# Optimization experiments

Hardware: AMD Instinct MI355X
Metric: run time of the kernel (lower is better)

## Reference

```python
import jax, jax.numpy as jnp
import numpy as np

NHEAD = 8
STRIP = 7  # strip_width (horizontal strips, is_vertical=False)


def setup_inputs() -> dict:
    key = jax.random.key(0)
    k0, k1, k2 = jax.random.split(key, 3)
    B, H, W, C = 2, 112, 112, 256
    x = jax.random.normal(k0, (B, H * W, C), dtype=jnp.float32)
    # torch nn.Linear weights: (out_features, in_features)
    qkv_w = jax.random.normal(k1, (3 * C, C), dtype=jnp.float32) * 0.02
    proj_w = jax.random.normal(k2, (C, C), dtype=jnp.float32) * 0.02
    proj_b = jnp.zeros((C,), dtype=jnp.float32)
    return {"x": x, "qkv_w": qkv_w, "proj_w": proj_w, "proj_b": proj_b,
            "H_feat": 112, "W_feat": 112}


def reference(x, qkv_w, proj_w, proj_b, H_feat, W_feat):
    B, N, C = x.shape
    hd = C // NHEAD
    scale = hd ** -0.5
    n_strips = H_feat // STRIP
    L = STRIP * W_feat  # tokens per horizontal strip
    # window_partition with window (STRIP, W_feat): nwW==1, so a pure reshape
    xs = x.reshape(B * n_strips, L, C)
    # qkv projection (Linear: y = x @ W^T), then split q/k/v and heads
    qkv = jnp.einsum('bnc,dc->bnd', xs, qkv_w)
    qkv = qkv.reshape(B * n_strips, L, 3, NHEAD, hd)
    q, k, v = jnp.moveaxis(qkv, 2, 0)  # each (Bw, L, H, hd)
    attn = jnp.einsum('bnhd,bmhd->bhnm', q * scale, k)
    attn = jax.nn.softmax(attn, axis=-1)
    out = jnp.einsum('bhnm,bmhd->bnhd', attn, v).reshape(B * n_strips, L, C)
    out = jnp.einsum('bnc,dc->bnd', out, proj_w) + proj_b
    # window_reverse is again a pure reshape for horizontal strips
    return out.reshape(B, N, C)
```

## Files before the change

### kernel.cpp

```cpp
#include <hip/hip_runtime.h>
#include <hip/hip_bf16.h>

#define M_ROWS 25088
#define CDIM   256
#define QKVD   768
#define LWIN   784
#define NWINH  256

typedef __attribute__((ext_vector_type(8))) short short8v;
typedef __attribute__((ext_vector_type(4))) float floatx4;

static __device__ __forceinline__ float bfs2f(unsigned short s) {
    return __uint_as_float(((unsigned int)s) << 16);
}
static __device__ __forceinline__ unsigned short f2bf(float f) {
    unsigned int x = __float_as_uint(f);
    x += 0x7fffu + ((x >> 16) & 1u);
    return (unsigned short)(x >> 16);
}
static __device__ __forceinline__ unsigned int cvt_pk_bf16(float a, float b) {
    unsigned int r;
    asm("v_cvt_pk_bf16_f32 %0, %1, %2" : "=v"(r) : "v"(a), "v"(b));
    return r;
}
static __device__ __forceinline__ void gld_lds16(const unsigned short* g,
                                                 unsigned short* l) {
    __builtin_amdgcn_global_load_lds(
        (const __attribute__((address_space(1))) unsigned int*)g,
        (__attribute__((address_space(3))) unsigned int*)l, 16, 0, 0);
}

__global__ __launch_bounds__(256) void k_f2bf(
    const float* __restrict__ src, unsigned short* __restrict__ dst, int n8)
{
    const float4* s4 = (const float4*)src;
    uint4* d4 = (uint4*)dst;
    for (int i = blockIdx.x * 256 + threadIdx.x; i < n8;
         i += gridDim.x * 256) {
        float4 a = s4[2 * i], b = s4[2 * i + 1];
        uint4 o;
        o.x = cvt_pk_bf16(a.x, a.y);
        o.y = cvt_pk_bf16(a.z, a.w);
        o.z = cvt_pk_bf16(b.x, b.y);
        o.w = cvt_pk_bf16(b.z, b.w);
        d4[i] = o;
    }
}

template <typename OUT_T, bool BIAS>
__global__ __launch_bounds__(256, 2) void k_gemm_mfma(
    const unsigned short* __restrict__ A,
    const unsigned short* __restrict__ B,
    const float* __restrict__ bias,
    OUT_T* __restrict__ Y, int N)
{
    __shared__ __attribute__((aligned(16))) unsigned short As[128 * 64];
    __shared__ __attribute__((aligned(16))) unsigned short Bs[128 * 64];
    const int t = threadIdx.x;
    const int lane = t & 63, wv = t >> 6;
    const int lq = lane & 15, g = lane >> 4;
    const int wm = wv >> 1, wn = wv & 1;
    const int R0 = blockIdx.y * 128, C0 = blockIdx.x * 128;
    const int lrow = t >> 3, lch = (t & 7) * 8;

    floatx4 acc[4][4];
#pragma unroll
    for (int i = 0; i < 4; ++i)
#pragma unroll
        for (int j = 0; j < 4; ++j) acc[i][j] = (floatx4){0.f, 0.f, 0.f, 0.f};

    for (int kc = 0; kc < 256; kc += 64) {
#pragma unroll
        for (int i = 0; i < 4; ++i) {
            gld_lds16(A + (size_t)(R0 + i * 32 + lrow) * 256 + kc + lch,
                      As + (i * 32 + wv * 8) * 64);
            gld_lds16(B + (size_t)(C0 + i * 32 + lrow) * 256 + kc + lch,
                      Bs + (i * 32 + wv * 8) * 64);
        }
        __syncthreads();
#pragma unroll
        for (int kk = 0; kk < 64; kk += 32) {
            short8v af[4], bf[4];
#pragma unroll
            for (int mi = 0; mi < 4; ++mi)
                af[mi] = *(const short8v*)(As + (wm * 64 + mi * 16 + lq) * 64 +
                                           kk + g * 8);
#pragma unroll
            for (int ni = 0; ni < 4; ++ni)
                bf[ni] = *(const short8v*)(Bs + (wn * 64 + ni * 16 + lq) * 64 +
                                           kk + g * 8);
#pragma unroll
            for (int mi = 0; mi < 4; ++mi)
#pragma unroll
                for (int ni = 0; ni < 4; ++ni)
                    acc[mi][ni] = __builtin_amdgcn_mfma_f32_16x16x32_bf16(
                        af[mi], bf[ni], acc[mi][ni], 0, 0, 0);
        }
        __syncthreads();
    }

#pragma unroll
    for (int mi = 0; mi < 4; ++mi) {
        const size_t rb = (size_t)R0 + wm * 64 + mi * 16 + g * 4;
#pragma unroll
        for (int ni = 0; ni < 4; ++ni) {
            const int col = C0 + wn * 64 + ni * 16 + lq;
            float bv = 0.f;
            if constexpr (BIAS) bv = bias[col];
#pragma unroll
            for (int r = 0; r < 4; ++r) {
                float val = acc[mi][ni][r] + bv;
                if constexpr (sizeof(OUT_T) == 2)
                    Y[(rb + r) * N + col] = (OUT_T)f2bf(val);
                else
                    Y[(rb + r) * N + col] = (OUT_T)val;
            }
        }
    }
}

#define VTP 808
#define KS_SZ (LWIN * 32)
#define VT_SZ (32 * VTP)
#define PB_OFF (KS_SZ + VT_SZ)
#define ATTN_LDS ((PB_OFF + 8 * 1280) * 2)

__global__ __launch_bounds__(512, 1) void k_attn_mfma(
    const unsigned short* __restrict__ qkv,
    unsigned short* __restrict__ ao)
{
    extern __shared__ unsigned short sm[];
    unsigned short* Ks = sm;
    unsigned short* Vt = sm + KS_SZ;
    const int t = threadIdx.x;
    const int lane = t & 63, wave = t >> 6;
    const int lq = lane & 15, g = lane >> 4;
    const int h = blockIdx.x & 7, w = blockIdx.x >> 3;
    const size_t rowbase = (size_t)w * LWIN;
    const unsigned short* base = qkv + rowbase * QKVD;

    for (int idx = t; idx < LWIN * 4; idx += 512) {
        const int row = idx >> 2, c = idx & 3;
        const size_t rb = (size_t)row * QKVD;
        uint4 kv = *(const uint4*)(base + rb + 256 + h * 32 + c * 8);
        *(uint4*)(Ks + c * (LWIN * 8) + row * 8) = kv;
        union { uint4 u; unsigned short s[8]; } vv;
        vv.u = *(const uint4*)(base + rb + 512 + h * 32 + c * 8);
#pragma unroll
        for (int j = 0; j < 8; ++j) Vt[(c * 8 + j) * VTP + row] = vv.s[j];
    }
    for (int idx = t; idx < 32 * 24; idx += 512) {
        Vt[(idx / 24) * VTP + LWIN + (idx % 24)] = 0;
    }
    __syncthreads();

    unsigned short* Pw = sm + PB_OFF + wave * 1280;
    const float CE = 1.4426950408889634f * 0.17677669529663687f;

    for (int c = wave; c < 25; c += 8) {
        const int tile0 = c * 2;
        const int nt = (c == 24) ? 1 : 2;
        short8v qf[2];
#pragma unroll
        for (int n = 0; n < 2; ++n)
            if (n < nt)
                qf[n] = *(const short8v*)(base +
                        (size_t)((tile0 + n) * 16 + lq) * QKVD + h * 32 + g * 8);

        floatx4 oa[2][2] = {{{0.f,0.f,0.f,0.f},{0.f,0.f,0.f,0.f}},
                            {{0.f,0.f,0.f,0.f},{0.f,0.f,0.f,0.f}}};
        float lsum[2] = {0.f, 0.f};

        auto do_score = [&](int s) {
            short8v kf = *(const short8v*)(Ks + g * (LWIN * 8) +
                                           (size_t)(s * 16 + lq) * 8);
#pragma unroll
            for (int n = 0; n < 2; ++n) {
                if (n < nt) {
                    floatx4 st = __builtin_amdgcn_mfma_f32_16x16x32_bf16(
                        kf, qf[n], (floatx4){0.f, 0.f, 0.f, 0.f}, 0, 0, 0);
                    float p0 = __builtin_amdgcn_exp2f(st[0] * CE);
                    float p1 = __builtin_amdgcn_exp2f(st[1] * CE);
                    float p2 = __builtin_amdgcn_exp2f(st[2] * CE);
                    float p3 = __builtin_amdgcn_exp2f(st[3] * CE);
                    lsum[n] += (p0 + p1) + (p2 + p3);
                    uint2 pw;
                    pw.x = cvt_pk_bf16(p0, p1);
                    pw.y = cvt_pk_bf16(p2, p3);
                    *(uint2*)(Pw + n * 640 + lq * 40 + (s & 1) * 16 + g * 4) = pw;
                }
            }
        };
        auto do_pv = [&](int tokbase) {
            short8v v0 = *(const short8v*)(Vt + (size_t)lq * VTP + tokbase + g * 8);
            short8v v1 = *(const short8v*)(Vt + (size_t)(lq + 16) * VTP + tokbase + g * 8);
#pragma unroll
            for (int n = 0; n < 2; ++n) {
                if (n < nt) {
                    short8v pf = *(const short8v*)(Pw + n * 640 + lq * 40 + g * 8);
                    oa[n][0] = __builtin_amdgcn_mfma_f32_16x16x32_bf16(
                        pf, v0, oa[n][0], 0, 0, 0);
                    oa[n][1] = __builtin_amdgcn_mfma_f32_16x16x32_bf16(
                        pf, v1, oa[n][1], 0, 0, 0);
                }
            }
        };

        for (int u = 0; u < 24; ++u) {
            do_score(2 * u);
            do_score(2 * u + 1);
            do_pv(u * 32);
        }
        do_score(48);
#pragma unroll
        for (int n = 0; n < 2; ++n) {
            if (n < nt) {
                uint2 z; z.x = 0u; z.y = 0u;
                *(uint2*)(Pw + n * 640 + lq * 40 + 16 + g * 4) = z;
            }
        }
        do_pv(768);

#pragma unroll
        for (int n = 0; n < 2; ++n) {
            if (n < nt) {
                float l = lsum[n];
                l += __shfl_xor(l, 16);
                l += __shfl_xor(l, 32);
                float inv = 1.f / l;
                const size_t orow0 = rowbase + (size_t)(tile0 + n) * 16;
#pragma unroll
                for (int r = 0; r < 4; ++r) {
                    float ir = __shfl(inv, (lane & 48) | (g * 4 + r));
                    size_t ob = (orow0 + g * 4 + r) * CDIM + h * 32;
                    ao[ob + lq]      = f2bf(oa[n][0][r] * ir);
                    ao[ob + 16 + lq] = f2bf(oa[n][1][r] * ir);
                }
            }
        }
    }
}

extern "C" void kernel_launch(void* const* d_in, const int* in_sizes, int n_in,
                              void* d_out, int out_size, void* d_ws, size_t ws_size,
                              hipStream_t stream) {
    const float* x      = (const float*)d_in[0];
    const float* qkv_w  = (const float*)d_in[1];
    const float* proj_w = (const float*)d_in[2];
    const float* proj_b = (const float*)d_in[3];
    float* out = (float*)d_out;

    unsigned short* qkvb = (unsigned short*)d_ws;
    unsigned short* xb   = qkvb + (size_t)M_ROWS * QKVD;
    unsigned short* aob  = xb;
    unsigned short* wqb  = xb + (size_t)M_ROWS * CDIM;
    unsigned short* wpb  = wqb + (size_t)QKVD * CDIM;

    hipFuncSetAttribute((const void*)k_attn_mfma,
                        hipFuncAttributeMaxDynamicSharedMemorySize, ATTN_LDS);

    k_f2bf<<<2048, 256, 0, stream>>>(x, xb, (M_ROWS * CDIM) / 8);
    k_f2bf<<<96, 256, 0, stream>>>(qkv_w, wqb, (QKVD * CDIM) / 8);
    k_f2bf<<<32, 256, 0, stream>>>(proj_w, wpb, (CDIM * CDIM) / 8);

    k_gemm_mfma<unsigned short, false>
        <<<dim3(QKVD / 128, M_ROWS / 128), 256, 0, stream>>>(
            xb, wqb, nullptr, qkvb, QKVD);

    k_attn_mfma<<<dim3(NWINH), 512, ATTN_LDS, stream>>>(qkvb, aob);

    k_gemm_mfma<float, true>
        <<<dim3(CDIM / 128, M_ROWS / 128), 256, 0, stream>>>(
            aob, wpb, proj_b, out, CDIM);
}
```

Measured before the change: 98.70 us.

## Use 16 waves per attention block with pair-packed V transpose and pre-scaled Q

The attention kernel now launches 1024 threads, and each of 16 waves handles one 16-row query tile instead of two tiles per wave across 8 waves. The score/PV loop is software-pipelined with a double-buffered P tile. V is transposed into LDS as 32-bit token pairs, which halves the scattered 16-bit LDS stores. The softmax scale times log2(e) is folded into the Q columns in the QKV GEMM epilogue, which removes a multiply per score. The cost is more LDS per block, higher register pressure under the 1024-thread bound, and Q being rounded to bf16 after scaling.

```diff
diff --git a/kernel.cpp b/kernel.cpp
--- a/kernel.cpp
+++ b/kernel.cpp
@@ -9,6 +9,8 @@
 
 typedef __attribute__((ext_vector_type(8))) short short8v;
 typedef __attribute__((ext_vector_type(4))) float floatx4;
+
+#define CEQ 0.2550660106245232f
 
 static __device__ __forceinline__ float bfs2f(unsigned short s) {
     return __uint_as_float(((unsigned int)s) << 16);
@@ -47,7 +49,7 @@
     }
 }
 
-template <typename OUT_T, bool BIAS>
+template <typename OUT_T, bool BIAS, bool SCALEQ>
 __global__ __launch_bounds__(256, 2) void k_gemm_mfma(
     const unsigned short* __restrict__ A,
     const unsigned short* __restrict__ B,
@@ -109,7 +111,9 @@
             if constexpr (BIAS) bv = bias[col];
 #pragma unroll
             for (int r = 0; r < 4; ++r) {
-                float val = acc[mi][ni][r] + bv;
+                float val = acc[mi][ni][r];
+                if constexpr (SCALEQ) { if (col < 256) val *= CEQ; }
+                val += bv;
                 if constexpr (sizeof(OUT_T) == 2)
                     Y[(rb + r) * N + col] = (OUT_T)f2bf(val);
                 else
@@ -119,19 +123,19 @@
     }
 }
 
-#define VTP 808
+#define VTP32 404
 #define KS_SZ (LWIN * 32)
-#define VT_SZ (32 * VTP)
-#define PB_OFF (KS_SZ + VT_SZ)
-#define ATTN_LDS ((PB_OFF + 8 * 1280) * 2)
-
-__global__ __launch_bounds__(512, 1) void k_attn_mfma(
+#define VT_SH (2 * 32 * VTP32)
+#define PB_OFF (KS_SZ + VT_SH)
+#define ATTN_LDS ((PB_OFF + 16 * 1280) * 2)
+
+__global__ __launch_bounds__(1024, 1) void k_attn_mfma(
     const unsigned short* __restrict__ qkv,
     unsigned short* __restrict__ ao)
 {
     extern __shared__ unsigned short sm[];
     unsigned short* Ks = sm;
-    unsigned short* Vt = sm + KS_SZ;
+    unsigned int*   Vt = (unsigned int*)(sm + KS_SZ);
     const int t = threadIdx.x;
     const int lane = t & 63, wave = t >> 6;
     const int lq = lane & 15, g = lane >> 4;
@@ -139,104 +143,86 @@
     const size_t rowbase = (size_t)w * LWIN;
     const unsigned short* base = qkv + rowbase * QKVD;
 
-    for (int idx = t; idx < LWIN * 4; idx += 512) {
+    for (int idx = t; idx < LWIN * 4; idx += 1024) {
         const int row = idx >> 2, c = idx & 3;
-        const size_t rb = (size_t)row * QKVD;
-        uint4 kv = *(const uint4*)(base + rb + 256 + h * 32 + c * 8);
+        uint4 kv = *(const uint4*)(base + (size_t)row * QKVD + 256 + h * 32 + c * 8);
         *(uint4*)(Ks + c * (LWIN * 8) + row * 8) = kv;
-        union { uint4 u; unsigned short s[8]; } vv;
-        vv.u = *(const uint4*)(base + rb + 512 + h * 32 + c * 8);
-#pragma unroll
-        for (int j = 0; j < 8; ++j) Vt[(c * 8 + j) * VTP + row] = vv.s[j];
-    }
-    for (int idx = t; idx < 32 * 24; idx += 512) {
-        Vt[(idx / 24) * VTP + LWIN + (idx % 24)] = 0;
+    }
+    for (int idx = t; idx < 392 * 4; idx += 1024) {
+        const int rp = idx >> 2, c = idx & 3;
+        union { uint4 u; unsigned short s[8]; } a, b;
+        a.u = *(const uint4*)(base + (size_t)(2 * rp) * QKVD + 512 + h * 32 + c * 8);
+        b.u = *(const uint4*)(base + (size_t)(2 * rp + 1) * QKVD + 512 + h * 32 + c * 8);
+#pragma unroll
+        for (int j = 0; j < 8; ++j)
+            Vt[(c * 8 + j) * VTP32 + rp] =
+                (unsigned int)a.s[j] | ((unsigned int)b.s[j] << 16);
+    }
+    for (int idx = t; idx < 32 * 12; idx += 1024) {
+        Vt[(idx / 12) * VTP32 + 392 + (idx % 12)] = 0;
     }
     __syncthreads();
 
     unsigned short* Pw = sm + PB_OFF + wave * 1280;
-    const float CE = 1.4426950408889634f * 0.17677669529663687f;
-
-    for (int c = wave; c < 25; c += 8) {
-        const int tile0 = c * 2;
-        const int nt = (c == 24) ? 1 : 2;
-        short8v qf[2];
-#pragma unroll
-        for (int n = 0; n < 2; ++n)
-            if (n < nt)
-                qf[n] = *(const short8v*)(base +
-                        (size_t)((tile0 + n) * 16 + lq) * QKVD + h * 32 + g * 8);
-
-        floatx4 oa[2][2] = {{{0.f,0.f,0.f,0.f},{0.f,0.f,0.f,0.f}},
-                            {{0.f,0.f,0.f,0.f},{0.f,0.f,0.f,0.f}}};
-        float lsum[2] = {0.f, 0.f};
-
-        auto do_score = [&](int s) {
+
+    for (int tq = wave; tq < 49; tq += 16) {
+        const short8v qf = *(const short8v*)(base +
+                (size_t)(tq * 16 + lq) * QKVD + h * 32 + g * 8);
+        floatx4 oa0 = {0.f, 0.f, 0.f, 0.f}, oa1 = {0.f, 0.f, 0.f, 0.f};
+        float lsum = 0.f;
+
+        auto score = [&](int s, int buf) {
             short8v kf = *(const short8v*)(Ks + g * (LWIN * 8) +
                                            (size_t)(s * 16 + lq) * 8);
-#pragma unroll
-            for (int n = 0; n < 2; ++n) {
-                if (n < nt) {
-                    floatx4 st = __builtin_amdgcn_mfma_f32_16x16x32_bf16(
-                        kf, qf[n], (floatx4){0.f, 0.f, 0.f, 0.f}, 0, 0, 0);
-                    float p0 = __builtin_amdgcn_exp2f(st[0] * CE);
-                    float p1 = __builtin_amdgcn_exp2f(st[1] * CE);
-                    float p2 = __builtin_amdgcn_exp2f(st[2] * CE);
-                    float p3 = __builtin_amdgcn_exp2f(st[3] * CE);
-                    lsum[n] += (p0 + p1) + (p2 + p3);
-                    uint2 pw;
-                    pw.x = cvt_pk_bf16(p0, p1);
-                    pw.y = cvt_pk_bf16(p2, p3);
-                    *(uint2*)(Pw + n * 640 + lq * 40 + (s & 1) * 16 + g * 4) = pw;
-                }
-            }
+            floatx4 st = __builtin_amdgcn_mfma_f32_16x16x32_bf16(
+                kf, qf, (floatx4){0.f, 0.f, 0.f, 0.f}, 0, 0, 0);
+            float p0 = __builtin_amdgcn_exp2f(st[0]);
+            float p1 = __builtin_amdgcn_exp2f(st[1]);
+            float p2 = __builtin_amdgcn_exp2f(st[2]);
+            float p3 = __builtin_amdgcn_exp2f(st[3]);
+            lsum += (p0 + p1) + (p2 + p3);
+            uint2 pw;
+            pw.x = cvt_pk_bf16(p0, p1);
+            pw.y = cvt_pk_bf16(p2, p3);
+            *(uint2*)(Pw + buf * 640 + lq * 40 + (s & 1) * 16 + g * 4) = pw;
         };
-        auto do_pv = [&](int tokbase) {
-            short8v v0 = *(const short8v*)(Vt + (size_t)lq * VTP + tokbase + g * 8);
-            short8v v1 = *(const short8v*)(Vt + (size_t)(lq + 16) * VTP + tokbase + g * 8);
-#pragma unroll
-            for (int n = 0; n < 2; ++n) {
-                if (n < nt) {
-                    short8v pf = *(const short8v*)(Pw + n * 640 + lq * 40 + g * 8);
-                    oa[n][0] = __builtin_amdgcn_mfma_f32_16x16x32_bf16(
-                        pf, v0, oa[n][0], 0, 0, 0);
-                    oa[n][1] = __builtin_amdgcn_mfma_f32_16x16x32_bf16(
-                        pf, v1, oa[n][1], 0, 0, 0);
-                }
-            }
+        auto pv = [&](int u) {
+            const int woff = u * 16;
+            short8v v0 = *(const short8v*)(const unsigned short*)(
+                Vt + (size_t)lq * VTP32 + woff + g * 4);
+            short8v v1 = *(const short8v*)(const unsigned short*)(
+                Vt + (size_t)(lq + 16) * VTP32 + woff + g * 4);
+            short8v pf = *(const short8v*)(Pw + (u & 1) * 640 + lq * 40 + g * 8);
+            oa0 = __builtin_amdgcn_mfma_f32_16x16x32_bf16(pf, v0, oa0, 0, 0, 0);
+            oa1 = __builtin_amdgcn_mfma_f32_16x16x32_bf16(pf, v1, oa1, 0, 0, 0);
         };
 
-        for (int u = 0; u < 24; ++u) {
-            do_score(2 * u);
-            do_score(2 * u + 1);
-            do_pv(u * 32);
-        }
-        do_score(48);
-#pragma unroll
-        for (int n = 0; n < 2; ++n) {
-            if (n < nt) {
-                uint2 z; z.x = 0u; z.y = 0u;
-                *(uint2*)(Pw + n * 640 + lq * 40 + 16 + g * 4) = z;
-            }
-        }
-        do_pv(768);
-
-#pragma unroll
-        for (int n = 0; n < 2; ++n) {
-            if (n < nt) {
-                float l = lsum[n];
-                l += __shfl_xor(l, 16);
-                l += __shfl_xor(l, 32);
-                float inv = 1.f / l;
-                const size_t orow0 = rowbase + (size_t)(tile0 + n) * 16;
-#pragma unroll
-                for (int r = 0; r < 4; ++r) {
-                    float ir = __shfl(inv, (lane & 48) | (g * 4 + r));
-                    size_t ob = (orow0 + g * 4 + r) * CDIM + h * 32;
-                    ao[ob + lq]      = f2bf(oa[n][0][r] * ir);
-                    ao[ob + 16 + lq] = f2bf(oa[n][1][r] * ir);
-                }
-            }
+        score(0, 0);
+        score(1, 0);
+        for (int u = 1; u < 24; ++u) {
+            score(2 * u, u & 1);
+            pv(u - 1);
+            score(2 * u + 1, u & 1);
+        }
+        score(48, 0);
+        pv(23);
+        {
+            uint2 z; z.x = 0u; z.y = 0u;
+            *(uint2*)(Pw + lq * 40 + 16 + g * 4) = z;
+        }
+        pv(24);
+
+        float l = lsum;
+        l += __shfl_xor(l, 16);
+        l += __shfl_xor(l, 32);
+        float inv = 1.f / l;
+        const size_t orow0 = rowbase + (size_t)tq * 16;
+#pragma unroll
+        for (int r = 0; r < 4; ++r) {
+            float ir = __shfl(inv, (lane & 48) | (g * 4 + r));
+            size_t ob = (orow0 + g * 4 + r) * CDIM + h * 32;
+            ao[ob + lq]      = f2bf(oa0[r] * ir);
+            ao[ob + 16 + lq] = f2bf(oa1[r] * ir);
         }
     }
 }
@@ -263,13 +249,13 @@
     k_f2bf<<<96, 256, 0, stream>>>(qkv_w, wqb, (QKVD * CDIM) / 8);
     k_f2bf<<<32, 256, 0, stream>>>(proj_w, wpb, (CDIM * CDIM) / 8);
 
-    k_gemm_mfma<unsigned short, false>
+    k_gemm_mfma<unsigned short, false, true>
         <<<dim3(QKVD / 128, M_ROWS / 128), 256, 0, stream>>>(
             xb, wqb, nullptr, qkvb, QKVD);
 
-    k_attn_mfma<<<dim3(NWINH), 512, ATTN_LDS, stream>>>(qkvb, aob);
-
-    k_gemm_mfma<float, true>
+    k_attn_mfma<<<dim3(NWINH), 1024, ATTN_LDS, stream>>>(qkvb, aob);
+
+    k_gemm_mfma<float, true, false>
         <<<dim3(CDIM / 128, M_ROWS / 128), 256, 0, stream>>>(
             aob, wpb, proj_b, out, CDIM);
 }
```

Result: faster. 90.35 us (-8.5%).
